# Kernel optimization log

Hardware: AMD Instinct MI355X
Metric: run time of the kernel (lower is better)

The kernel has to match this reference:

```python
import jax, jax.numpy as jnp
import numpy as np

B, Q, K, H, DV = 16, 256, 256, 256, 256


def setup_inputs() -> dict:
    key = jax.random.key(0)
    ks = jax.random.split(key, 6)
    return {
        "queries": jax.random.normal(ks[0], (B, Q, H), dtype=jnp.float32),
        "keys": jax.random.normal(ks[1], (B, K, H), dtype=jnp.float32),
        "values": jax.random.normal(ks[2], (B, K, DV), dtype=jnp.float32),
        "W_q": jax.random.normal(ks[3], (H, H), dtype=jnp.float32) / np.sqrt(H),
        "W_k": jax.random.normal(ks[4], (H, H), dtype=jnp.float32) / np.sqrt(H),
        "w_v": jax.random.normal(ks[5], (H,), dtype=jnp.float32) / np.sqrt(H),
    }


def reference(queries, keys, values, W_q, W_k, w_v):
    # Linear projections (nn.Linear: x @ W.T), bias-free
    q = jnp.einsum("bqd,hd->bqh", queries, W_q)  # [B,Q,H]
    k = jnp.einsum("bkd,hd->bkh", keys, W_k)      # [B,K,H]
    # Broadcast add -> tanh -> scalar projection
    features = jnp.tanh(q[:, :, None, :] + k[:, None, :, :])  # [B,Q,K,H]
    scores = jnp.einsum("bqkh,h->bqk", features, w_v)          # [B,Q,K]
    attn = jax.nn.softmax(scores, axis=-1)                      # [B,Q,K]
    return jnp.einsum("bqk,bkv->bqv", attn, values)            # [B,Q,DV]
```

## Files before the change

### kernel.cpp

```cpp
#include <hip/hip_runtime.h>

#define Bn 16
#define Qn 256
#define Kn 256
#define Hn 256
#define DVn 256

constexpr float C2    = 2.8853900817779268f;
constexpr float LOG2E = 1.4426950408889634f;

__device__ __forceinline__ float fast_exp2(float x) { return __builtin_amdgcn_exp2f(x); }
__device__ __forceinline__ float fast_rcp(float x)  { return __builtin_amdgcn_rcpf(x); }

__device__ __forceinline__ unsigned short f2bf(float x) {
    unsigned u = __float_as_uint(x);
    u += 0x7fffu + ((u >> 16) & 1u);
    return (unsigned short)(u >> 16);
}

__global__ __launch_bounds__(256)
void proj_exp_kernel(const float* __restrict__ q, const float* __restrict__ kx,
                     const float* __restrict__ wq, const float* __restrict__ wk,
                     const float* __restrict__ V,
                     float* __restrict__ Eq, unsigned short* __restrict__ Ekb,
                     float* __restrict__ Vp)
{
    const int z = blockIdx.z;
    const int tid = threadIdx.x;
    if (z == 2) {
        const int L = blockIdx.y * 4 + blockIdx.x;
        #pragma unroll
        for (int j = 0; j < 4; ++j) {
            const int p   = L * 1024 + j * 256 + tid;
            const int bk4 = p >> 8;
            const int dv  = p & 255;
            const int b   = bk4 >> 6, k4 = bk4 & 63;
            const float* src = V + ((size_t)(b * Kn + 4 * k4)) * DVn + dv;
            float4 o;
            o.x = src[0 * DVn]; o.y = src[1 * DVn]; o.z = src[2 * DVn]; o.w = src[3 * DVn];
            *(float4*)(Vp + (size_t)p * 4) = o;
        }
        return;
    }
    const float* A = z ? kx : q;
    const float* W = z ? wk : wq;
    const int m0 = blockIdx.y * 64;
    const int n0 = blockIdx.x * 64;
    __shared__ __align__(16) float As[2][16][68];
    __shared__ __align__(16) float Bs[2][16][68];
    const int tx = tid & 15, ty = tid >> 4;
    const int lr = tid >> 2, lk4 = (tid & 3) * 4;
    const float* Arow = A + (size_t)(m0 + lr) * Hn + lk4;
    const float* Wrow = W + (size_t)(n0 + lr) * Hn + lk4;
    {
        float4 a = *(const float4*)(Arow);
        float4 w = *(const float4*)(Wrow);
        As[0][lk4+0][lr] = a.x; As[0][lk4+1][lr] = a.y; As[0][lk4+2][lr] = a.z; As[0][lk4+3][lr] = a.w;
        Bs[0][lk4+0][lr] = w.x; Bs[0][lk4+1][lr] = w.y; Bs[0][lk4+2][lr] = w.z; Bs[0][lk4+3][lr] = w.w;
    }
    __syncthreads();
    float acc[4][4] = {};
    int cur = 0;
    for (int k0 = 0; k0 < Hn; k0 += 16) {
        float4 an, wn;
        const bool more = (k0 + 16 < Hn);
        if (more) {
            an = *(const float4*)(Arow + k0 + 16);
            wn = *(const float4*)(Wrow + k0 + 16);
        }
        #pragma unroll
        for (int kk = 0; kk < 16; ++kk) {
            float4 av = *(const float4*)&As[cur][kk][ty*4];
            float4 bv = *(const float4*)&Bs[cur][kk][tx*4];
            const float ar[4] = {av.x, av.y, av.z, av.w};
            const float br[4] = {bv.x, bv.y, bv.z, bv.w};
            #pragma unroll
            for (int i = 0; i < 4; ++i)
                #pragma unroll
                for (int j = 0; j < 4; ++j)
                    acc[i][j] = fmaf(ar[i], br[j], acc[i][j]);
        }
        if (more) {
            const int nxt = cur ^ 1;
            As[nxt][lk4+0][lr] = an.x; As[nxt][lk4+1][lr] = an.y; As[nxt][lk4+2][lr] = an.z; As[nxt][lk4+3][lr] = an.w;
            Bs[nxt][lk4+0][lr] = wn.x; Bs[nxt][lk4+1][lr] = wn.y; Bs[nxt][lk4+2][lr] = wn.z; Bs[nxt][lk4+3][lr] = wn.w;
            __syncthreads();
            cur = nxt;
        }
    }
    #pragma unroll
    for (int i = 0; i < 4; ++i) {
        float4 o;
        o.x = fast_exp2(C2 * acc[i][0]);
        o.y = fast_exp2(C2 * acc[i][1]);
        o.z = fast_exp2(C2 * acc[i][2]);
        o.w = fast_exp2(C2 * acc[i][3]);
        if (z == 0) {
            *(float4*)(Eq + (size_t)(m0 + ty*4 + i) * Hn + n0 + tx*4) = o;
        } else {
            const int m  = m0 + ty*4 + i;
            const int bq = m >> 8, kk2 = m & 255;
            const int hg = (n0 + tx*4) >> 2;
            ushort4 s;
            s.x = f2bf(o.x); s.y = f2bf(o.y); s.z = f2bf(o.z); s.w = f2bf(o.w);
            *(ushort4*)(Ekb + ((size_t)(bq * 64 + hg) * 256 + kk2) * 4) = s;
        }
    }
}

__global__ __launch_bounds__(256)
void fused_attn_kernel(const float* __restrict__ Eq, const unsigned short* __restrict__ Ekb,
                       const float* __restrict__ wv, const float* __restrict__ Vp,
                       float* __restrict__ out)
{
    const int b  = blockIdx.y;
    const int q0 = blockIdx.x * 8;
    __shared__ __align__(16) float sEq[8 * 256];
    __shared__ __align__(16) float swv[256];
    __shared__ __align__(16) float sP[8 * 260];
    __shared__ float sredM[8][4];
    __shared__ float sredS[8][4];
    const int tid = threadIdx.x;
    #pragma unroll
    for (int r = 0; r < 2; ++r) {
        const int i = tid + r * 256;
        const int qq = i >> 6, h4 = (i & 63) * 4;
        *(float4*)&sEq[qq*256 + h4] = *(const float4*)(Eq + (size_t)(b*Qn + q0 + qq) * Hn + h4);
    }
    swv[tid] = wv[tid];
    __syncthreads();

    float sc[8] = {};
    const uint2* ekp = (const uint2*)Ekb + (size_t)b * 16384 + tid;
    uint2 e[4];
    #pragma unroll
    for (int g = 0; g < 4; ++g) e[g] = ekp[g * 256];
    for (int it = 0; it < 16; ++it) {
        uint2 en[4];
        if (it < 15) {
            #pragma unroll
            for (int g = 0; g < 4; ++g) en[g] = ekp[(4*(it+1) + g) * 256];
        }
        const int h0 = it * 16;
        float ek[16];
        #pragma unroll
        for (int g = 0; g < 4; ++g) {
            ek[4*g+0] = __uint_as_float(e[g].x << 16);
            ek[4*g+1] = __uint_as_float(e[g].x & 0xFFFF0000u);
            ek[4*g+2] = __uint_as_float(e[g].y << 16);
            ek[4*g+3] = __uint_as_float(e[g].y & 0xFFFF0000u);
        }
        #pragma unroll
        for (int qq = 0; qq < 8; ++qq) {
            float a = sc[qq];
            #pragma unroll
            for (int g = 0; g < 4; ++g) {
                const float4 ea = *(const float4*)&sEq[qq*256 + h0 + 4*g];
                const float4 wa = *(const float4*)&swv[h0 + 4*g];
                a = fmaf(wa.x, fast_rcp(fmaf(ea.x, ek[4*g+0], 1.f)), a);
                a = fmaf(wa.y, fast_rcp(fmaf(ea.y, ek[4*g+1], 1.f)), a);
                a = fmaf(wa.z, fast_rcp(fmaf(ea.z, ek[4*g+2], 1.f)), a);
                a = fmaf(wa.w, fast_rcp(fmaf(ea.w, ek[4*g+3], 1.f)), a);
            }
            sc[qq] = a;
        }
        #pragma unroll
        for (int g = 0; g < 4; ++g) e[g] = en[g];
    }

    const int w = tid >> 6, lane = tid & 63;
    #pragma unroll
    for (int qq = 0; qq < 8; ++qq) {
        sc[qq] = -2.0f * sc[qq];
        float mx = sc[qq];
        #pragma unroll
        for (int off = 32; off; off >>= 1) mx = fmaxf(mx, __shfl_xor(mx, off, 64));
        if (lane == 0) sredM[qq][w] = mx;
    }
    __syncthreads();
    #pragma unroll
    for (int qq = 0; qq < 8; ++qq) {
        const float mx = fmaxf(fmaxf(sredM[qq][0], sredM[qq][1]),
                               fmaxf(sredM[qq][2], sredM[qq][3]));
        const float p = fast_exp2(LOG2E * (sc[qq] - mx));
        float s = p;
        #pragma unroll
        for (int off = 32; off; off >>= 1) s += __shfl_xor(s, off, 64);
        if (lane == 0) sredS[qq][w] = s;
        sP[qq*260 + tid] = p;
    }
    __syncthreads();
    float rinv[8];
    #pragma unroll
    for (int qq = 0; qq < 8; ++qq)
        rinv[qq] = fast_rcp(sredS[qq][0] + sredS[qq][1] + sredS[qq][2] + sredS[qq][3]);

    float acc[8] = {};
    const float4* vp = (const float4*)Vp + (size_t)b * 64 * 256 + tid;
    float4 vv = vp[0];
    for (int k4 = 0; k4 < 64; ++k4) {
        float4 vn;
        if (k4 < 63) vn = vp[(k4 + 1) * 256];
        #pragma unroll
        for (int qq = 0; qq < 8; ++qq) {
            const float4 pq = *(const float4*)&sP[qq*260 + 4*k4];
            float a = acc[qq];
            a = fmaf(pq.x, vv.x, a);
            a = fmaf(pq.y, vv.y, a);
            a = fmaf(pq.z, vv.z, a);
            a = fmaf(pq.w, vv.w, a);
            acc[qq] = a;
        }
        vv = vn;
    }
    float* ob = out + (size_t)(b*Qn + q0) * DVn + tid;
    #pragma unroll
    for (int qq = 0; qq < 8; ++qq)
        ob[(size_t)qq * DVn] = acc[qq] * rinv[qq];
}

extern "C" void kernel_launch(void* const* d_in, const int* in_sizes, int n_in,
                              void* d_out, int out_size, void* d_ws, size_t ws_size,
                              hipStream_t stream) {
    const float* queries = (const float*)d_in[0];
    const float* keys    = (const float*)d_in[1];
    const float* values  = (const float*)d_in[2];
    const float* W_q     = (const float*)d_in[3];
    const float* W_k     = (const float*)d_in[4];
    const float* w_v     = (const float*)d_in[5];
    float* out = (float*)d_out;

    float*          Eq  = (float*)d_ws;
    unsigned short* Ekb = (unsigned short*)(Eq + (size_t)Bn * Qn * Hn);
    float*          Vp  = (float*)(Ekb + (size_t)Bn * Kn * Hn);

    proj_exp_kernel<<<dim3(4, 64, 3), 256, 0, stream>>>(queries, keys, W_q, W_k, values,
                                                        Eq, Ekb, Vp);
    fused_attn_kernel<<<dim3(32, 16), 256, 0, stream>>>(Eq, Ekb, w_v, Vp, out);
}
```

Measured before the change: 138.4 us.

## Use packed FP32 FMA with Newton reciprocal and halve queries per block

Replaces the scalar hardware reciprocal in the score loop with a bit-trick initial guess plus two Newton iterations, run on packed two-wide FMA. The goal is to move the transcendental-unit-bound rcp work onto the packed FMA path. The projection GEMM and the P·V loop also switch to packed FMA. The attention kernel now handles 4 queries per block instead of 8 with twice as many blocks, so each block does less work but the Ek tile is re-read by more blocks. The Newton reciprocal costs extra FMAs and gives slightly different accuracy than the hardware rcp.

```diff
diff --git a/kernel.cpp b/kernel.cpp
--- a/kernel.cpp
+++ b/kernel.cpp
@@ -9,13 +9,31 @@
 constexpr float C2    = 2.8853900817779268f;
 constexpr float LOG2E = 1.4426950408889634f;
 
+typedef float v2f __attribute__((ext_vector_type(2)));
+
 __device__ __forceinline__ float fast_exp2(float x) { return __builtin_amdgcn_exp2f(x); }
 __device__ __forceinline__ float fast_rcp(float x)  { return __builtin_amdgcn_rcpf(x); }
+__device__ __forceinline__ v2f pk_fma(v2f a, v2f b, v2f c) {
+    return __builtin_elementwise_fma(a, b, c);
+}
 
 __device__ __forceinline__ unsigned short f2bf(float x) {
     unsigned u = __float_as_uint(x);
     u += 0x7fffu + ((u >> 16) & 1u);
     return (unsigned short)(u >> 16);
+}
+
+__device__ __forceinline__ v2f pk_rcp(v2f x) {
+    uint2 u = __builtin_bit_cast(uint2, x);
+    u.x = 0x7EF311C3u - u.x;
+    u.y = 0x7EF311C3u - u.y;
+    v2f y = __builtin_bit_cast(v2f, u);
+    const v2f two = {2.0f, 2.0f};
+    v2f t = pk_fma(-x, y, two);
+    y = y * t;
+    t = pk_fma(-x, y, two);
+    y = y * t;
+    return y;
 }
 
 __global__ __launch_bounds__(256)
@@ -59,7 +77,7 @@
         Bs[0][lk4+0][lr] = w.x; Bs[0][lk4+1][lr] = w.y; Bs[0][lk4+2][lr] = w.z; Bs[0][lk4+3][lr] = w.w;
     }
     __syncthreads();
-    float acc[4][4] = {};
+    v2f acc2[4][2] = {};
     int cur = 0;
     for (int k0 = 0; k0 < Hn; k0 += 16) {
         float4 an, wn;
@@ -72,13 +90,15 @@
         for (int kk = 0; kk < 16; ++kk) {
             float4 av = *(const float4*)&As[cur][kk][ty*4];
             float4 bv = *(const float4*)&Bs[cur][kk][tx*4];
+            const v2f b01 = {bv.x, bv.y};
+            const v2f b23 = {bv.z, bv.w};
             const float ar[4] = {av.x, av.y, av.z, av.w};
-            const float br[4] = {bv.x, bv.y, bv.z, bv.w};
             #pragma unroll
-            for (int i = 0; i < 4; ++i)
-                #pragma unroll
-                for (int j = 0; j < 4; ++j)
-                    acc[i][j] = fmaf(ar[i], br[j], acc[i][j]);
+            for (int i = 0; i < 4; ++i) {
+                const v2f ai = {ar[i], ar[i]};
+                acc2[i][0] = pk_fma(ai, b01, acc2[i][0]);
+                acc2[i][1] = pk_fma(ai, b23, acc2[i][1]);
+            }
         }
         if (more) {
             const int nxt = cur ^ 1;
@@ -91,10 +111,10 @@
     #pragma unroll
     for (int i = 0; i < 4; ++i) {
         float4 o;
-        o.x = fast_exp2(C2 * acc[i][0]);
-        o.y = fast_exp2(C2 * acc[i][1]);
-        o.z = fast_exp2(C2 * acc[i][2]);
-        o.w = fast_exp2(C2 * acc[i][3]);
+        o.x = fast_exp2(C2 * acc2[i][0].x);
+        o.y = fast_exp2(C2 * acc2[i][0].y);
+        o.z = fast_exp2(C2 * acc2[i][1].x);
+        o.w = fast_exp2(C2 * acc2[i][1].y);
         if (z == 0) {
             *(float4*)(Eq + (size_t)(m0 + ty*4 + i) * Hn + n0 + tx*4) = o;
         } else {
@@ -114,23 +134,22 @@
                        float* __restrict__ out)
 {
     const int b  = blockIdx.y;
-    const int q0 = blockIdx.x * 8;
-    __shared__ __align__(16) float sEq[8 * 256];
+    const int q0 = blockIdx.x * 4;
+    __shared__ __align__(16) float sEq[4 * 256];
     __shared__ __align__(16) float swv[256];
-    __shared__ __align__(16) float sP[8 * 260];
-    __shared__ float sredM[8][4];
-    __shared__ float sredS[8][4];
+    __shared__ __align__(16) float sPv[256 * 4];
+    __shared__ float sredM[4][4];
+    __shared__ float sredS[4][4];
     const int tid = threadIdx.x;
-    #pragma unroll
-    for (int r = 0; r < 2; ++r) {
-        const int i = tid + r * 256;
-        const int qq = i >> 6, h4 = (i & 63) * 4;
+    {
+        const int qq = tid >> 6, h4 = (tid & 63) * 4;
         *(float4*)&sEq[qq*256 + h4] = *(const float4*)(Eq + (size_t)(b*Qn + q0 + qq) * Hn + h4);
-    }
-    swv[tid] = wv[tid];
-    __syncthreads();
-
-    float sc[8] = {};
+        swv[tid] = wv[tid];
+    }
+    __syncthreads();
+
+    const v2f one = {1.0f, 1.0f};
+    v2f acc2[4] = {};
     const uint2* ekp = (const uint2*)Ekb + (size_t)b * 16384 + tid;
     uint2 e[4];
     #pragma unroll
@@ -142,81 +161,83 @@
             for (int g = 0; g < 4; ++g) en[g] = ekp[(4*(it+1) + g) * 256];
         }
         const int h0 = it * 16;
-        float ek[16];
+        v2f eklo[4], ekhi[4];
         #pragma unroll
         for (int g = 0; g < 4; ++g) {
-            ek[4*g+0] = __uint_as_float(e[g].x << 16);
-            ek[4*g+1] = __uint_as_float(e[g].x & 0xFFFF0000u);
-            ek[4*g+2] = __uint_as_float(e[g].y << 16);
-            ek[4*g+3] = __uint_as_float(e[g].y & 0xFFFF0000u);
-        }
-        #pragma unroll
-        for (int qq = 0; qq < 8; ++qq) {
-            float a = sc[qq];
+            eklo[g] = v2f{__uint_as_float(e[g].x << 16), __uint_as_float(e[g].x & 0xFFFF0000u)};
+            ekhi[g] = v2f{__uint_as_float(e[g].y << 16), __uint_as_float(e[g].y & 0xFFFF0000u)};
+        }
+        #pragma unroll
+        for (int qq = 0; qq < 4; ++qq) {
+            v2f a = acc2[qq];
             #pragma unroll
             for (int g = 0; g < 4; ++g) {
                 const float4 ea = *(const float4*)&sEq[qq*256 + h0 + 4*g];
                 const float4 wa = *(const float4*)&swv[h0 + 4*g];
-                a = fmaf(wa.x, fast_rcp(fmaf(ea.x, ek[4*g+0], 1.f)), a);
-                a = fmaf(wa.y, fast_rcp(fmaf(ea.y, ek[4*g+1], 1.f)), a);
-                a = fmaf(wa.z, fast_rcp(fmaf(ea.z, ek[4*g+2], 1.f)), a);
-                a = fmaf(wa.w, fast_rcp(fmaf(ea.w, ek[4*g+3], 1.f)), a);
+                const v2f eq01 = {ea.x, ea.y}, eq23 = {ea.z, ea.w};
+                const v2f w01  = {wa.x, wa.y}, w23  = {wa.z, wa.w};
+                v2f x = pk_fma(eq01, eklo[g], one);
+                a = pk_fma(w01, pk_rcp(x), a);
+                x = pk_fma(eq23, ekhi[g], one);
+                a = pk_fma(w23, pk_rcp(x), a);
             }
-            sc[qq] = a;
+            acc2[qq] = a;
         }
         #pragma unroll
         for (int g = 0; g < 4; ++g) e[g] = en[g];
     }
 
     const int w = tid >> 6, lane = tid & 63;
-    #pragma unroll
-    for (int qq = 0; qq < 8; ++qq) {
-        sc[qq] = -2.0f * sc[qq];
-        float mx = sc[qq];
+    float s4[4];
+    #pragma unroll
+    for (int qq = 0; qq < 4; ++qq) {
+        s4[qq] = -2.0f * (acc2[qq].x + acc2[qq].y);
+        float mx = s4[qq];
         #pragma unroll
         for (int off = 32; off; off >>= 1) mx = fmaxf(mx, __shfl_xor(mx, off, 64));
         if (lane == 0) sredM[qq][w] = mx;
     }
     __syncthreads();
-    #pragma unroll
-    for (int qq = 0; qq < 8; ++qq) {
+    float pq[4];
+    #pragma unroll
+    for (int qq = 0; qq < 4; ++qq) {
         const float mx = fmaxf(fmaxf(sredM[qq][0], sredM[qq][1]),
                                fmaxf(sredM[qq][2], sredM[qq][3]));
-        const float p = fast_exp2(LOG2E * (sc[qq] - mx));
-        float s = p;
+        pq[qq] = fast_exp2(LOG2E * (s4[qq] - mx));
+        float s = pq[qq];
         #pragma unroll
         for (int off = 32; off; off >>= 1) s += __shfl_xor(s, off, 64);
         if (lane == 0) sredS[qq][w] = s;
-        sP[qq*260 + tid] = p;
-    }
-    __syncthreads();
-    float rinv[8];
-    #pragma unroll
-    for (int qq = 0; qq < 8; ++qq)
+    }
+    *(float4*)&sPv[tid * 4] = make_float4(pq[0], pq[1], pq[2], pq[3]);
+    __syncthreads();
+    float rinv[4];
+    #pragma unroll
+    for (int qq = 0; qq < 4; ++qq)
         rinv[qq] = fast_rcp(sredS[qq][0] + sredS[qq][1] + sredS[qq][2] + sredS[qq][3]);
 
-    float acc[8] = {};
+    v2f accP0 = {0.f, 0.f}, accP1 = {0.f, 0.f};
     const float4* vp = (const float4*)Vp + (size_t)b * 64 * 256 + tid;
     float4 vv = vp[0];
     for (int k4 = 0; k4 < 64; ++k4) {
         float4 vn;
         if (k4 < 63) vn = vp[(k4 + 1) * 256];
-        #pragma unroll
-        for (int qq = 0; qq < 8; ++qq) {
-            const float4 pq = *(const float4*)&sP[qq*260 + 4*k4];
-            float a = acc[qq];
-            a = fmaf(pq.x, vv.x, a);
-            a = fmaf(pq.y, vv.y, a);
-            a = fmaf(pq.z, vv.z, a);
-            a = fmaf(pq.w, vv.w, a);
-            acc[qq] = a;
+        const float vj[4] = {vv.x, vv.y, vv.z, vv.w};
+        #pragma unroll
+        for (int j = 0; j < 4; ++j) {
+            const float4 p4 = *(const float4*)&sPv[(4*k4 + j) * 4];
+            const v2f p01 = {p4.x, p4.y}, p23 = {p4.z, p4.w};
+            const v2f vb = {vj[j], vj[j]};
+            accP0 = pk_fma(p01, vb, accP0);
+            accP1 = pk_fma(p23, vb, accP1);
         }
         vv = vn;
     }
     float* ob = out + (size_t)(b*Qn + q0) * DVn + tid;
-    #pragma unroll
-    for (int qq = 0; qq < 8; ++qq)
-        ob[(size_t)qq * DVn] = acc[qq] * rinv[qq];
+    ob[0 * DVn] = accP0.x * rinv[0];
+    ob[1 * DVn] = accP0.y * rinv[1];
+    ob[2 * DVn] = accP1.x * rinv[2];
+    ob[3 * DVn] = accP1.y * rinv[3];
 }
 
 extern "C" void kernel_launch(void* const* d_in, const int* in_sizes, int n_in,
@@ -236,5 +257,5 @@
 
     proj_exp_kernel<<<dim3(4, 64, 3), 256, 0, stream>>>(queries, keys, W_q, W_k, values,
                                                         Eq, Ekb, Vp);
-    fused_attn_kernel<<<dim3(32, 16), 256, 0, stream>>>(Eq, Ekb, w_v, Vp, out);
-}
+    fused_attn_kernel<<<dim3(64, 16), 256, 0, stream>>>(Eq, Ekb, w_v, Vp, out);
+}
```

After: 138.2 us. No clear change (-0.1%).

## Use bf16 MFMA for projections and shrink attention blocks to four queries

Applied to the files above, without the earlier changes.

Adds a prep kernel that converts queries, keys and both weight matrices to bf16, alongside the existing V transpose. The fp32 shared-memory SGEMM is replaced by a kernel built on 16x16x32 bf16 MFMA instructions. The attention kernel now handles four queries per block instead of eight, doubling the grid, and reads Eq and w_v straight from global memory instead of staging them in LDS. The trade-offs are an extra launch, lower projection precision before the exp, and scattered scalar stores in the MFMA epilogue.

```diff
diff --git a/kernel.cpp b/kernel.cpp
--- a/kernel.cpp
+++ b/kernel.cpp
@@ -1,4 +1,5 @@
 #include <hip/hip_runtime.h>
+#include <hip/hip_fp16.h>
 
 #define Bn 16
 #define Qn 256
@@ -9,6 +10,9 @@
 constexpr float C2    = 2.8853900817779268f;
 constexpr float LOG2E = 1.4426950408889634f;
 
+typedef __attribute__((ext_vector_type(8))) short bf16x8;
+typedef __attribute__((ext_vector_type(4))) float f32x4;
+
 __device__ __forceinline__ float fast_exp2(float x) { return __builtin_amdgcn_exp2f(x); }
 __device__ __forceinline__ float fast_rcp(float x)  { return __builtin_amdgcn_rcpf(x); }
 
@@ -19,91 +23,88 @@
 }
 
 __global__ __launch_bounds__(256)
-void proj_exp_kernel(const float* __restrict__ q, const float* __restrict__ kx,
-                     const float* __restrict__ wq, const float* __restrict__ wk,
-                     const float* __restrict__ V,
-                     float* __restrict__ Eq, unsigned short* __restrict__ Ekb,
-                     float* __restrict__ Vp)
+void prep_kernel(const float* __restrict__ q, const float* __restrict__ kx,
+                 const float* __restrict__ wq, const float* __restrict__ wk,
+                 const float* __restrict__ V,
+                 unsigned short* __restrict__ Xb, unsigned short* __restrict__ Wb,
+                 float* __restrict__ Vp)
 {
-    const int z = blockIdx.z;
-    const int tid = threadIdx.x;
-    if (z == 2) {
-        const int L = blockIdx.y * 4 + blockIdx.x;
-        #pragma unroll
-        for (int j = 0; j < 4; ++j) {
-            const int p   = L * 1024 + j * 256 + tid;
-            const int bk4 = p >> 8;
-            const int dv  = p & 255;
-            const int b   = bk4 >> 6, k4 = bk4 & 63;
-            const float* src = V + ((size_t)(b * Kn + 4 * k4)) * DVn + dv;
-            float4 o;
-            o.x = src[0 * DVn]; o.y = src[1 * DVn]; o.z = src[2 * DVn]; o.w = src[3 * DVn];
-            *(float4*)(Vp + (size_t)p * 4) = o;
-        }
-        return;
-    }
-    const float* A = z ? kx : q;
-    const float* W = z ? wk : wq;
-    const int m0 = blockIdx.y * 64;
-    const int n0 = blockIdx.x * 64;
-    __shared__ __align__(16) float As[2][16][68];
-    __shared__ __align__(16) float Bs[2][16][68];
-    const int tx = tid & 15, ty = tid >> 4;
-    const int lr = tid >> 2, lk4 = (tid & 3) * 4;
-    const float* Arow = A + (size_t)(m0 + lr) * Hn + lk4;
-    const float* Wrow = W + (size_t)(n0 + lr) * Hn + lk4;
+    const int g = blockIdx.x * 256 + threadIdx.x;
     {
-        float4 a = *(const float4*)(Arow);
-        float4 w = *(const float4*)(Wrow);
-        As[0][lk4+0][lr] = a.x; As[0][lk4+1][lr] = a.y; As[0][lk4+2][lr] = a.z; As[0][lk4+3][lr] = a.w;
-        Bs[0][lk4+0][lr] = w.x; Bs[0][lk4+1][lr] = w.y; Bs[0][lk4+2][lr] = w.z; Bs[0][lk4+3][lr] = w.w;
-    }
-    __syncthreads();
-    float acc[4][4] = {};
-    int cur = 0;
-    for (int k0 = 0; k0 < Hn; k0 += 16) {
-        float4 an, wn;
-        const bool more = (k0 + 16 < Hn);
-        if (more) {
-            an = *(const float4*)(Arow + k0 + 16);
-            wn = *(const float4*)(Wrow + k0 + 16);
-        }
-        #pragma unroll
-        for (int kk = 0; kk < 16; ++kk) {
-            float4 av = *(const float4*)&As[cur][kk][ty*4];
-            float4 bv = *(const float4*)&Bs[cur][kk][tx*4];
-            const float ar[4] = {av.x, av.y, av.z, av.w};
-            const float br[4] = {bv.x, bv.y, bv.z, bv.w};
-            #pragma unroll
-            for (int i = 0; i < 4; ++i)
-                #pragma unroll
-                for (int j = 0; j < 4; ++j)
-                    acc[i][j] = fmaf(ar[i], br[j], acc[i][j]);
-        }
-        if (more) {
-            const int nxt = cur ^ 1;
-            As[nxt][lk4+0][lr] = an.x; As[nxt][lk4+1][lr] = an.y; As[nxt][lk4+2][lr] = an.z; As[nxt][lk4+3][lr] = an.w;
-            Bs[nxt][lk4+0][lr] = wn.x; Bs[nxt][lk4+1][lr] = wn.y; Bs[nxt][lk4+2][lr] = wn.z; Bs[nxt][lk4+3][lr] = wn.w;
-            __syncthreads();
-            cur = nxt;
-        }
-    }
-    #pragma unroll
-    for (int i = 0; i < 4; ++i) {
+        const float* xs = (g < 131072) ? (q + (size_t)g * 8)
+                                       : (kx + (size_t)(g - 131072) * 8);
+        float4 x0 = *(const float4*)xs;
+        float4 x1 = *(const float4*)(xs + 4);
+        ushort4 o0, o1;
+        o0.x = f2bf(x0.x); o0.y = f2bf(x0.y); o0.z = f2bf(x0.z); o0.w = f2bf(x0.w);
+        o1.x = f2bf(x1.x); o1.y = f2bf(x1.y); o1.z = f2bf(x1.z); o1.w = f2bf(x1.w);
+        *(ushort4*)(Xb + (size_t)g * 8)     = o0;
+        *(ushort4*)(Xb + (size_t)g * 8 + 4) = o1;
+    }
+    if (g < 32768) {
+        const float* ws = (g < 16384) ? (wq + (size_t)g * 4)
+                                      : (wk + (size_t)(g - 16384) * 4);
+        float4 w0 = *(const float4*)ws;
+        ushort4 o;
+        o.x = f2bf(w0.x); o.y = f2bf(w0.y); o.z = f2bf(w0.z); o.w = f2bf(w0.w);
+        *(ushort4*)(Wb + (size_t)g * 4) = o;
+    }
+    {
+        const int p   = g;
+        const int bk4 = p >> 8, dv = p & 255;
+        const int b   = bk4 >> 6, k4 = bk4 & 63;
+        const float* src = V + ((size_t)(b * Kn + 4 * k4)) * DVn + dv;
         float4 o;
-        o.x = fast_exp2(C2 * acc[i][0]);
-        o.y = fast_exp2(C2 * acc[i][1]);
-        o.z = fast_exp2(C2 * acc[i][2]);
-        o.w = fast_exp2(C2 * acc[i][3]);
-        if (z == 0) {
-            *(float4*)(Eq + (size_t)(m0 + ty*4 + i) * Hn + n0 + tx*4) = o;
-        } else {
-            const int m  = m0 + ty*4 + i;
-            const int bq = m >> 8, kk2 = m & 255;
-            const int hg = (n0 + tx*4) >> 2;
-            ushort4 s;
-            s.x = f2bf(o.x); s.y = f2bf(o.y); s.z = f2bf(o.z); s.w = f2bf(o.w);
-            *(ushort4*)(Ekb + ((size_t)(bq * 64 + hg) * 256 + kk2) * 4) = s;
+        o.x = src[0 * DVn]; o.y = src[1 * DVn]; o.z = src[2 * DVn]; o.w = src[3 * DVn];
+        *(float4*)(Vp + (size_t)p * 4) = o;
+    }
+}
+
+__global__ __launch_bounds__(256)
+void proj_mfma_kernel(const unsigned short* __restrict__ Xb,
+                      const unsigned short* __restrict__ Wb,
+                      float* __restrict__ Eq, unsigned short* __restrict__ Ekb)
+{
+    const int tid  = threadIdx.x;
+    const int wvid = tid >> 6, lane = tid & 63;
+    const int m0   = blockIdx.x * 16;
+    const int n0   = wvid * 64;
+    const bool isQ = (m0 < 4096);
+    const int r16  = lane & 15, q8 = (lane >> 4) * 8;
+
+    const unsigned short* Xrow  = Xb + (size_t)(m0 + r16) * 256 + q8;
+    const unsigned short* Wbase = Wb + (isQ ? 0 : 65536);
+
+    bf16x8 afr[8];
+    #pragma unroll
+    for (int s = 0; s < 8; ++s) afr[s] = *(const bf16x8*)(Xrow + s * 32);
+
+    f32x4 acc[4];
+    #pragma unroll
+    for (int nt = 0; nt < 4; ++nt) {
+        const unsigned short* Wrow = Wbase + (size_t)(n0 + nt * 16 + r16) * 256 + q8;
+        f32x4 c = {0.f, 0.f, 0.f, 0.f};
+        #pragma unroll
+        for (int s = 0; s < 8; ++s) {
+            bf16x8 bfr = *(const bf16x8*)(Wrow + s * 32);
+            c = __builtin_amdgcn_mfma_f32_16x16x32_bf16(afr[s], bfr, c, 0, 0, 0);
+        }
+        acc[nt] = c;
+    }
+    const int rbase = (lane >> 4) * 4;
+    #pragma unroll
+    for (int nt = 0; nt < 4; ++nt) {
+        const int n = n0 + nt * 16 + r16;
+        #pragma unroll
+        for (int r = 0; r < 4; ++r) {
+            const int m = m0 + rbase + r;
+            const float val = fast_exp2(C2 * acc[nt][r]);
+            if (isQ) {
+                Eq[(size_t)m * 256 + n] = val;
+            } else {
+                const int kr = m - 4096, b = kr >> 8, kk = kr & 255;
+                Ekb[(((size_t)(b * 64 + (n >> 2))) * 256 + kk) * 4 + (n & 3)] = f2bf(val);
+            }
         }
     }
 }
@@ -114,23 +115,15 @@
                        float* __restrict__ out)
 {
     const int b  = blockIdx.y;
-    const int q0 = blockIdx.x * 8;
-    __shared__ __align__(16) float sEq[8 * 256];
-    __shared__ __align__(16) float swv[256];
-    __shared__ __align__(16) float sP[8 * 260];
-    __shared__ float sredM[8][4];
-    __shared__ float sredS[8][4];
+    const int q0 = blockIdx.x * 4;
+    __shared__ __align__(16) float sPv[256 * 4];
+    __shared__ float sredM[4][4];
+    __shared__ float sredS[4][4];
     const int tid = threadIdx.x;
-    #pragma unroll
-    for (int r = 0; r < 2; ++r) {
-        const int i = tid + r * 256;
-        const int qq = i >> 6, h4 = (i & 63) * 4;
-        *(float4*)&sEq[qq*256 + h4] = *(const float4*)(Eq + (size_t)(b*Qn + q0 + qq) * Hn + h4);
-    }
-    swv[tid] = wv[tid];
-    __syncthreads();
-
-    float sc[8] = {};
+
+    const float* eq0 = Eq + (size_t)(b * Qn + q0) * Hn;
+
+    float sc[4] = {0.f, 0.f, 0.f, 0.f};
     const uint2* ekp = (const uint2*)Ekb + (size_t)b * 16384 + tid;
     uint2 e[4];
     #pragma unroll
@@ -139,7 +132,7 @@
         uint2 en[4];
         if (it < 15) {
             #pragma unroll
-            for (int g = 0; g < 4; ++g) en[g] = ekp[(4*(it+1) + g) * 256];
+            for (int g = 0; g < 4; ++g) en[g] = ekp[(4 * (it + 1) + g) * 256];
         }
         const int h0 = it * 16;
         float ek[16];
@@ -151,18 +144,18 @@
             ek[4*g+3] = __uint_as_float(e[g].y & 0xFFFF0000u);
         }
         #pragma unroll
-        for (int qq = 0; qq < 8; ++qq) {
-            float a = sc[qq];
+        for (int g = 0; g < 4; ++g) {
+            const float4 wa = *(const float4*)(wv + h0 + 4 * g);
             #pragma unroll
-            for (int g = 0; g < 4; ++g) {
-                const float4 ea = *(const float4*)&sEq[qq*256 + h0 + 4*g];
-                const float4 wa = *(const float4*)&swv[h0 + 4*g];
+            for (int qq = 0; qq < 4; ++qq) {
+                const float4 ea = *(const float4*)(eq0 + qq * 256 + h0 + 4 * g);
+                float a = sc[qq];
                 a = fmaf(wa.x, fast_rcp(fmaf(ea.x, ek[4*g+0], 1.f)), a);
                 a = fmaf(wa.y, fast_rcp(fmaf(ea.y, ek[4*g+1], 1.f)), a);
                 a = fmaf(wa.z, fast_rcp(fmaf(ea.z, ek[4*g+2], 1.f)), a);
                 a = fmaf(wa.w, fast_rcp(fmaf(ea.w, ek[4*g+3], 1.f)), a);
+                sc[qq] = a;
             }
-            sc[qq] = a;
         }
         #pragma unroll
         for (int g = 0; g < 4; ++g) e[g] = en[g];
@@ -170,7 +163,7 @@
 
     const int w = tid >> 6, lane = tid & 63;
     #pragma unroll
-    for (int qq = 0; qq < 8; ++qq) {
+    for (int qq = 0; qq < 4; ++qq) {
         sc[qq] = -2.0f * sc[qq];
         float mx = sc[qq];
         #pragma unroll
@@ -178,45 +171,46 @@
         if (lane == 0) sredM[qq][w] = mx;
     }
     __syncthreads();
-    #pragma unroll
-    for (int qq = 0; qq < 8; ++qq) {
+    float pq[4];
+    #pragma unroll
+    for (int qq = 0; qq < 4; ++qq) {
         const float mx = fmaxf(fmaxf(sredM[qq][0], sredM[qq][1]),
                                fmaxf(sredM[qq][2], sredM[qq][3]));
-        const float p = fast_exp2(LOG2E * (sc[qq] - mx));
-        float s = p;
+        pq[qq] = fast_exp2(LOG2E * (sc[qq] - mx));
+        float s = pq[qq];
         #pragma unroll
         for (int off = 32; off; off >>= 1) s += __shfl_xor(s, off, 64);
         if (lane == 0) sredS[qq][w] = s;
-        sP[qq*260 + tid] = p;
-    }
+    }
+    *(float4*)&sPv[tid * 4] = make_float4(pq[0], pq[1], pq[2], pq[3]);
     __syncthreads();
-    float rinv[8];
-    #pragma unroll
-    for (int qq = 0; qq < 8; ++qq)
+    float rinv[4];
+    #pragma unroll
+    for (int qq = 0; qq < 4; ++qq)
         rinv[qq] = fast_rcp(sredS[qq][0] + sredS[qq][1] + sredS[qq][2] + sredS[qq][3]);
 
-    float acc[8] = {};
+    float acc[4] = {0.f, 0.f, 0.f, 0.f};
     const float4* vp = (const float4*)Vp + (size_t)b * 64 * 256 + tid;
     float4 vv = vp[0];
     for (int k4 = 0; k4 < 64; ++k4) {
         float4 vn;
         if (k4 < 63) vn = vp[(k4 + 1) * 256];
-        #pragma unroll
-        for (int qq = 0; qq < 8; ++qq) {
-            const float4 pq = *(const float4*)&sP[qq*260 + 4*k4];
-            float a = acc[qq];
-            a = fmaf(pq.x, vv.x, a);
-            a = fmaf(pq.y, vv.y, a);
-            a = fmaf(pq.z, vv.z, a);
-            a = fmaf(pq.w, vv.w, a);
-            acc[qq] = a;
+        const float vj[4] = {vv.x, vv.y, vv.z, vv.w};
+        #pragma unroll
+        for (int j = 0; j < 4; ++j) {
+            const float4 p4 = *(const float4*)&sPv[(4 * k4 + j) * 4];
+            acc[0] = fmaf(p4.x, vj[j], acc[0]);
+            acc[1] = fmaf(p4.y, vj[j], acc[1]);
+            acc[2] = fmaf(p4.z, vj[j], acc[2]);
+            acc[3] = fmaf(p4.w, vj[j], acc[3]);
         }
         vv = vn;
     }
-    float* ob = out + (size_t)(b*Qn + q0) * DVn + tid;
-    #pragma unroll
-    for (int qq = 0; qq < 8; ++qq)
-        ob[(size_t)qq * DVn] = acc[qq] * rinv[qq];
+    float* ob = out + (size_t)(b * Qn + q0) * DVn + tid;
+    ob[0 * DVn] = acc[0] * rinv[0];
+    ob[1 * DVn] = acc[1] * rinv[1];
+    ob[2 * DVn] = acc[2] * rinv[2];
+    ob[3 * DVn] = acc[3] * rinv[3];
 }
 
 extern "C" void kernel_launch(void* const* d_in, const int* in_sizes, int n_in,
@@ -233,8 +227,11 @@
     float*          Eq  = (float*)d_ws;
     unsigned short* Ekb = (unsigned short*)(Eq + (size_t)Bn * Qn * Hn);
     float*          Vp  = (float*)(Ekb + (size_t)Bn * Kn * Hn);
-
-    proj_exp_kernel<<<dim3(4, 64, 3), 256, 0, stream>>>(queries, keys, W_q, W_k, values,
-                                                        Eq, Ekb, Vp);
-    fused_attn_kernel<<<dim3(32, 16), 256, 0, stream>>>(Eq, Ekb, w_v, Vp, out);
-}
+    unsigned short* Xb  = (unsigned short*)(Vp + (size_t)Bn * Kn * DVn);
+    unsigned short* Wb  = Xb + (size_t)2 * Bn * Qn * Hn;
+
+    prep_kernel<<<dim3(1024), 256, 0, stream>>>(queries, keys, W_q, W_k, values,
+                                                Xb, Wb, Vp);
+    proj_mfma_kernel<<<dim3(512), 256, 0, stream>>>(Xb, Wb, Eq, Ekb);
+    fused_attn_kernel<<<dim3(64, 16), 256, 0, stream>>>(Eq, Ekb, w_v, Vp, out);
+}
```

Result: faster. 128.9 us (-6.8%).
